# Kernel optimization log

Measured on AMD Instinct MI355X. Metric: run time of the kernel, lower is better.

## Reference

```python
import jax, jax.numpy as jnp
import numpy as np

B, N1, D, H = 64, 201, 128, 4
HALF = (N1 - 1) // 2  # 100 pickup/delivery pairs
V_RANGE = 6.0
NEG = -1e20


def _uni(key, shape):
    s = 1.0 / np.sqrt(shape[-1])
    return jax.random.uniform(key, shape, jnp.float32, -s, s)


def setup_inputs() -> dict:
    key = jax.random.key(0)
    ks = jax.random.split(key, 24)
    h_wave = jax.random.normal(ks[0], (B, N1, D), jnp.float32)
    # solution must be a valid permutation per batch (it is argsorted / self-gathered)
    solution = jax.vmap(lambda k: jax.random.permutation(k, N1))(jax.random.split(ks[1], B)).astype(jnp.int32)
    selection_recent = jax.random.uniform(ks[2], (B, 4, HALF), jnp.float32)
    pre_action = jax.random.randint(ks[3], (B, 2), 1, HALF).astype(jnp.int32)
    mask_table = jnp.zeros((B, N1, N1), dtype=bool)
    params = dict(
        Wn=_uni(ks[4], (D, D)), Wg=_uni(ks[5], (D, D)),
        rm_WQ=_uni(ks[6], (H, D, D)), rm_WK=_uni(ks[7], (H, D, D)),
        rm_w1=_uni(ks[8], (2 * H + 4, 32)), rm_b1=_uni(ks[9], (32,)),
        rm_w2=_uni(ks[10], (32, 32)), rm_b2=_uni(ks[11], (32,)),
        rm_w3=_uni(ks[12], (32, 1)), rm_b3=_uni(ks[13], (1,)),
        i1_Wq=_uni(ks[14], (H, D, D)), i1_Wk=_uni(ks[15], (H, D, D)),
        i2_Wq=_uni(ks[16], (H, D, D)), i2_Wk=_uni(ks[17], (H, D, D)),
        re_w1=_uni(ks[18], (4 * H, 32)), re_b1=_uni(ks[19], (32,)),
        re_w2=_uni(ks[20], (32, 32)), re_b2=_uni(ks[21], (32,)),
        re_w3=_uni(ks[22], (32, 1)), re_b3=_uni(ks[23], (1,)),
    )
    return dict(h_wave=h_wave, solution=solution, selection_recent=selection_recent,
                pre_action=pre_action, mask_table=mask_table, **params)


def _mlp(x, w1, b1, w2, b2, w3, b3):
    x = jax.nn.relu(x @ w1 + b1)
    x = jax.nn.relu(x @ w2 + b2)
    return (x @ w3 + b3)[..., 0]


def _mha_compat(q, k, Wq, Wk):
    # q: [B,Q,Din], k: [B,K,Din]; Wq/Wk: [H,Din,Dh] -> compat [H,B,Q,K]
    Q = jnp.einsum('bqd,hde->hbqe', q, Wq)
    K = jnp.einsum('bkd,hde->hbke', k, Wk)
    return jnp.einsum('hbqe,hbke->hbqk', Q, K) * (1.0 / np.sqrt(Wq.shape[-1]))


def _removal(h_hat, solution, selection_recent, WQ, WK, w1, b1, w2, b2, w3, b3):
    pre = jnp.argsort(solution, axis=1)
    post = jnp.take_along_axis(solution, solution, axis=1)
    hQ = jnp.einsum('bnd,hde->hbne', h_hat, WQ)  # [H,B,N1,D]
    hK = jnp.einsum('bnd,hde->hbne', h_hat, WK)
    Qpre = jnp.take_along_axis(hQ, pre[None, :, :, None], axis=2)
    Kpost = jnp.take_along_axis(hK, post[None, :, :, None], axis=2)
    comp = ((Qpre * hK).sum(-1) + (hQ * Kpost).sum(-1) - (Qpre * Kpost).sum(-1))[:, :, 1:]  # [H,B,N1-1]
    pairing = jnp.concatenate([comp[:, :, :N1 // 2], comp[:, :, N1 // 2:]], axis=0)  # [2H,B,HALF]
    feat = jnp.concatenate([jnp.transpose(pairing, (1, 2, 0)),
                            jnp.transpose(selection_recent, (0, 2, 1))], axis=-1)  # [B,HALF,2H+4]
    return _mlp(feat, w1, b1, w2, b2, w3, b3)  # [B,HALF]


def _reinsertion(h_hat, pos_pickup, pos_delivery, solution, Wq1, Wk1, Wq2, Wk2, w1, b1, w2, b2, w3, b3):
    ar = jnp.arange(B)
    h_p = h_hat[ar, pos_pickup][:, None, :]   # [B,1,D]
    h_d = h_hat[ar, pos_delivery][:, None, :]
    h_nb = jnp.take_along_axis(h_hat, solution[:, :, None], axis=1)  # [B,N1,D]

    def as_row(c):  # [H,B,1,N1] -> [B,N1,1,H] broadcast over columns
        return jnp.broadcast_to(jnp.transpose(c, (1, 2, 3, 0)).reshape(B, N1, 1, H), (B, N1, N1, H))

    def as_col(c):  # [H,B,1,N1] -> [B,1,N1,H] broadcast over rows
        return jnp.broadcast_to(jnp.transpose(c, (1, 2, 3, 0)).reshape(B, 1, N1, H), (B, N1, N1, H))

    feat = jnp.concatenate([
        as_row(_mha_compat(h_p, h_hat, Wq1, Wk1)),
        as_row(_mha_compat(h_p, h_nb, Wq2, Wk2)),
        as_col(_mha_compat(h_d, h_hat, Wq1, Wk1)),
        as_col(_mha_compat(h_d, h_nb, Wq2, Wk2)),
    ], axis=-1)  # [B,N1,N1,4H]
    return _mlp(feat, w1, b1, w2, b2, w3, b3)  # [B,N1,N1]


def _forward(h_wave, selection_recent, Wn, Wg, rm_WQ, rm_WK, rm_w1, rm_b1, rm_w2, rm_b2,
             rm_w3, rm_b3, i1_Wq, i1_Wk, i2_Wq, i2_Wk, re_w1, re_b1, re_w2, re_b2,
             re_w3, re_b3, solution, pre_action, mask_table):
    ar = jnp.arange(B)
    h_hat = h_wave @ Wn + (jnp.max(h_wave, axis=1) @ Wg)[:, None, :]
    t1 = jnp.tanh(_removal(h_hat, solution, selection_recent, rm_WQ, rm_WK,
                           rm_w1, rm_b1, rm_w2, rm_b2, rm_w3, rm_b3)) * V_RANGE
    t1 = jnp.where(pre_action[0, 0] > 0, t1.at[ar, pre_action[:, 0]].set(NEG), t1)
    logp1 = jax.nn.log_softmax(t1, axis=-1)
    a1 = jnp.argmax(t1, axis=-1)  # deterministic stand-in for Categorical sampling
    ll1 = jnp.take_along_axis(logp1, a1[:, None], axis=1)[:, 0]
    pos_pickup = 1 + a1
    pos_delivery = pos_pickup + HALF
    t2 = jnp.tanh(_reinsertion(h_hat, pos_pickup, pos_delivery, solution,
                               i1_Wq, i1_Wk, i2_Wq, i2_Wk,
                               re_w1, re_b1, re_w2, re_b2, re_w3, re_b3)) * V_RANGE
    t2 = jnp.where(mask_table, NEG, t2).reshape(B, N1 * N1)
    logp2 = jax.nn.log_softmax(t2, axis=-1)
    pair = jnp.argmax(t2, axis=-1)
    ll2 = jnp.take_along_axis(logp2, pair[:, None], axis=1)[:, 0]
    action = jnp.stack([a1, pair // N1, pair % N1], axis=-1)
    return action, ll1 + ll2


def reference(h_wave, solution, selection_recent, pre_action, mask_table,
              Wn, Wg, rm_WQ, rm_WK, rm_w1, rm_b1, rm_w2, rm_b2, rm_w3, rm_b3,
              i1_Wq, i1_Wk, i2_Wq, i2_Wk, re_w1, re_b1, re_w2, re_b2, re_w3, re_b3):
    return _forward(h_wave, selection_recent, Wn, Wg, rm_WQ, rm_WK, rm_w1, rm_b1,
                    rm_w2, rm_b2, rm_w3, rm_b3, i1_Wq, i1_Wk, i2_Wq, i2_Wk,
                    re_w1, re_b1, re_w2, re_b2, re_w3, re_b3,
                    solution, pre_action, mask_table)
```

## Files before the change

### kernel.cpp

```cpp
#include <hip/hip_runtime.h>
#include <math.h>

#define BB 64
#define N1 201
#define DD 128
#define HALF 100
#define NN (N1*N1)
#define NEGV (-1e20f)
#define QSCALE 0.08838834764831845f
#define NELE 1646592u

typedef __attribute__((ext_vector_type(8))) short short8v;
typedef __attribute__((ext_vector_type(4))) float float4v;

#define OFF_M    0u
#define OFF_MF   196608u
#define OFF_HWB  516096u
#define OFF_HHAT 2985984u
#define OFF_HBF  4632576u
#define OFF_G    7102464u
#define OFF_PMAX 7110656u
#define OFF_CMP  7143424u
#define OFF_Q    7194624u
#define OFF_ROWH 7325696u
#define OFF_COLH 7737344u
#define OFF_SC   8148992u
#define OFF_PM   8149248u
#define OFF_PS   8151296u
#define OFF_PI   8153344u
#define OFF_W2F  8155392u

__device__ __forceinline__ unsigned short f2bf(float x) {
    unsigned u = __float_as_uint(x);
    unsigned r = u + 0x7fffu + ((u >> 16) & 1u);
    return (unsigned short)(r >> 16);
}
__device__ __forceinline__ float bf2f(unsigned short h) {
    return __uint_as_float(((unsigned)h) << 16);
}

__global__ void kprep2(const float* __restrict__ rmWQ, const float* __restrict__ rmWK,
                       const float* __restrict__ i1Wq, const float* __restrict__ i1Wk,
                       const float* __restrict__ i2Wq, const float* __restrict__ i2Wk,
                       const float* __restrict__ re_w2, float* __restrict__ ws) {
    int m = blockIdx.x, jg = blockIdx.y, t = threadIdx.x;
    if (m == 12) {
        if (jg != 0) return;
        unsigned short* w2f = (unsigned short*)(ws + OFF_W2F);
        for (int idx = t; idx < 4*64*8; idx += 128) {
            int fs = idx >> 9, l = (idx >> 3) & 63, i = idx & 7;
            int j = 16*(fs >> 1) + (l & 15);
            int k = ((l >> 4) * 8) + i;
            float v = re_w2[k*32 + j];
            unsigned short hi = f2bf(v);
            unsigned short outv;
            if (fs & 1) outv = f2bf(v - bf2f(hi));
            else        outv = hi;
            w2f[idx] = outv;
        }
        return;
    }
    const float* WQ; const float* WK;
    if (m < 4)      { WQ = rmWQ + m*16384;     WK = rmWK + m*16384; }
    else if (m < 8) { WQ = i1Wq + (m-4)*16384; WK = i1Wk + (m-4)*16384; }
    else            { WQ = i2Wq + (m-8)*16384; WK = i2Wk + (m-8)*16384; }
    __shared__ float wq[128*132];
    __shared__ float wk[32*133];
    for (int idx = t; idx < 128*128; idx += 128) {
        int r = idx >> 7, e = idx & 127;
        wq[r*132 + e] = WQ[idx];
    }
    for (int idx = t; idx < 32*128; idx += 128) {
        int r = idx >> 7, e = idx & 127;
        wk[r*133 + e] = WK[(jg*32 + r)*128 + e];
    }
    __syncthreads();
    int j = t & 31, iq = t >> 5;
    for (int i2 = 0; i2 < 32; ++i2) {
        int i = iq*32 + i2;
        float acc = 0.f;
        #pragma unroll 8
        for (int e = 0; e < 128; ++e) acc += wq[i*132 + e]*wk[j*133 + e];
        ws[OFF_M + m*16384 + i*128 + jg*32 + j] = acc;
    }
}

__global__ void kfrag(const float* __restrict__ Wn, float* __restrict__ ws) {
    int bid = blockIdx.x;
    int mat = bid >> 5, rem = bid & 31, nt = rem >> 2, ks = rem & 3;
    const float* src = (mat < 12) ? (ws + OFF_M + mat*16384) : Wn;
    int l = threadIdx.x;
    unsigned short* mf = (unsigned short*)(ws + OFF_MF)
                       + (size_t)mat*49152 + (size_t)((nt*4 + ks)*3)*512 + l*8;
    #pragma unroll
    for (int i = 0; i < 8; ++i) {
        int k = ks*32 + (l >> 4)*8 + i;
        int col = nt*16 + (l & 15);
        float v = src[k*128 + col];
        unsigned short h = f2bf(v);
        float r1 = v - bf2f(h);
        unsigned short mm = f2bf(r1);
        unsigned short lo = f2bf(r1 - bf2f(mm));
        mf[i] = h; mf[512 + i] = mm; mf[1024 + i] = lo;
    }
}

__global__ void khw3(const float* __restrict__ hw, float* __restrict__ ws) {
    unsigned idx = blockIdx.x*256u + threadIdx.x;
    if (idx >= NELE) return;
    unsigned short* hh = (unsigned short*)(ws + OFF_HWB);
    unsigned short* hm = hh + NELE;
    unsigned short* hl = hh + 2u*NELE;
    float v = hw[idx];
    unsigned short a = f2bf(v);
    float r1 = v - bf2f(a);
    unsigned short b = f2bf(r1);
    unsigned short c = f2bf(r1 - bf2f(b));
    hh[idx] = a; hm[idx] = b; hl[idx] = c;
}

__global__ void kpartmax(const float* __restrict__ hw, float* __restrict__ pmax) {
    int b = blockIdx.x, p = blockIdx.y, d = threadIdx.x;
    int n0 = p*51, ne = n0 + 51; if (ne > N1) ne = N1;
    float m = -INFINITY;
    const float* src = hw + ((size_t)b*N1)*DD + d;
    for (int n = n0; n < ne; ++n) m = fmaxf(m, src[n*DD]);
    pmax[(b*4 + p)*128 + d] = m;
}

__global__ void khmaxg(const float* __restrict__ pmax, const float* __restrict__ Wg,
                       float* __restrict__ g) {
    int b = blockIdx.x, d = threadIdx.x;
    __shared__ float hm[128];
    const float* pm = pmax + b*4*128 + d;
    hm[d] = fmaxf(fmaxf(pm[0], pm[128]), fmaxf(pm[256], pm[384]));
    __syncthreads();
    float acc = 0.f;
    for (int k = 0; k < 128; ++k) acc += hm[k] * Wg[k*128 + d];
    g[b*128 + d] = acc;
}

__global__ __launch_bounds__(256) void khhat2(const float* __restrict__ g,
                                              float* __restrict__ ws) {
    int b = blockIdx.x, cg = blockIdx.y;
    int t = threadIdx.x, w = t >> 6, l = t & 63;
    const unsigned short* hwh = (const unsigned short*)(ws + OFF_HWB);
    const unsigned short* hwm = hwh + NELE;
    const unsigned short* hwl = hwh + 2u*NELE;
    const unsigned short* wnf = (const unsigned short*)(ws + OFF_MF) + (size_t)12*49152;
    float* hhat = ws + OFF_HHAT;
    unsigned short* hbh = (unsigned short*)(ws + OFF_HBF);
    unsigned short* hbm = hbh + NELE;
    unsigned short* hbl = hbh + 2u*NELE;
    int col0 = cg*32 + (l & 15);
    float g0 = g[b*128 + col0];
    float g1 = g[b*128 + col0 + 16];
    for (int mt = w; mt < 13; mt += 4) {
        int arow = mt*16 + (l & 15); if (arow > 200) arow = 200;
        size_t abase = ((size_t)b*N1 + arow)*DD;
        float4v acc0 = {g0, g0, g0, g0};
        float4v acc1 = {g1, g1, g1, g1};
        #pragma unroll
        for (int ks = 0; ks < 4; ++ks) {
            size_t ao = abase + ks*32 + (l >> 4)*8;
            short8v ah = *(const short8v*)(hwh + ao);
            short8v am = *(const short8v*)(hwm + ao);
            short8v al = *(const short8v*)(hwl + ao);
            const short8v* bf0 = (const short8v*)(wnf + (size_t)(((cg*2 + 0)*4 + ks)*3)*512) + l;
            const short8v* bf1 = (const short8v*)(wnf + (size_t)(((cg*2 + 1)*4 + ks)*3)*512) + l;
            short8v bh0 = bf0[0], bm0 = bf0[64], bl0 = bf0[128];
            short8v bh1 = bf1[0], bm1 = bf1[64], bl1 = bf1[128];
            acc0 = __builtin_amdgcn_mfma_f32_16x16x32_bf16(ah, bh0, acc0, 0, 0, 0);
            acc1 = __builtin_amdgcn_mfma_f32_16x16x32_bf16(ah, bh1, acc1, 0, 0, 0);
            acc0 = __builtin_amdgcn_mfma_f32_16x16x32_bf16(ah, bm0, acc0, 0, 0, 0);
            acc1 = __builtin_amdgcn_mfma_f32_16x16x32_bf16(ah, bm1, acc1, 0, 0, 0);
            acc0 = __builtin_amdgcn_mfma_f32_16x16x32_bf16(am, bh0, acc0, 0, 0, 0);
            acc1 = __builtin_amdgcn_mfma_f32_16x16x32_bf16(am, bh1, acc1, 0, 0, 0);
            acc0 = __builtin_amdgcn_mfma_f32_16x16x32_bf16(ah, bl0, acc0, 0, 0, 0);
            acc1 = __builtin_amdgcn_mfma_f32_16x16x32_bf16(ah, bl1, acc1, 0, 0, 0);
            acc0 = __builtin_amdgcn_mfma_f32_16x16x32_bf16(al, bh0, acc0, 0, 0, 0);
            acc1 = __builtin_amdgcn_mfma_f32_16x16x32_bf16(al, bh1, acc1, 0, 0, 0);
            acc0 = __builtin_amdgcn_mfma_f32_16x16x32_bf16(am, bm0, acc0, 0, 0, 0);
            acc1 = __builtin_amdgcn_mfma_f32_16x16x32_bf16(am, bm1, acc1, 0, 0, 0);
        }
        #pragma unroll
        for (int r = 0; r < 4; ++r) {
            int row = mt*16 + (l >> 4)*4 + r;
            if (row < N1) {
                size_t i0 = ((size_t)b*N1 + row)*DD + col0;
                float v0 = acc0[r], v1 = acc1[r];
                hhat[i0] = v0; hhat[i0 + 16] = v1;
                unsigned short a0 = f2bf(v0); float r10 = v0 - bf2f(a0);
                unsigned short b0 = f2bf(r10);
                hbh[i0] = a0; hbm[i0] = b0; hbl[i0] = f2bf(r10 - bf2f(b0));
                unsigned short a1 = f2bf(v1); float r11 = v1 - bf2f(a1);
                unsigned short b1 = f2bf(r11);
                hbh[i0+16] = a1; hbm[i0+16] = b1; hbl[i0+16] = f2bf(r11 - bf2f(b1));
            }
        }
    }
}

__global__ __launch_bounds__(256) void kAC(const int* __restrict__ solution,
                                           float* __restrict__ ws) {
    int b = blockIdx.x, h = blockIdx.y;
    int t = threadIdx.x, w = t >> 6, l = t & 63;
    __shared__ float As[N1*132];
    __shared__ int sol[N1], pre[N1], post[N1];
    if (t < N1) sol[t] = solution[b*N1 + t];
    __syncthreads();
    if (t < N1) { pre[sol[t]] = t; post[t] = sol[sol[t]]; }
    const unsigned short* hbh = (const unsigned short*)(ws + OFF_HBF);
    const unsigned short* hbm = hbh + NELE;
    const unsigned short* hbl = hbh + 2u*NELE;
    const unsigned short* mfm = (const unsigned short*)(ws + OFF_MF) + (size_t)h*49152;
    for (int mt = 0; mt < 13; ++mt) {
        int arow = mt*16 + (l & 15); if (arow > 200) arow = 200;
        size_t abase = ((size_t)b*N1 + arow)*DD;
        float4v acc0 = {0.f, 0.f, 0.f, 0.f};
        float4v acc1 = {0.f, 0.f, 0.f, 0.f};
        #pragma unroll
        for (int ks = 0; ks < 4; ++ks) {
            size_t ao = abase + ks*32 + (l >> 4)*8;
            short8v ah = *(const short8v*)(hbh + ao);
            short8v am = *(const short8v*)(hbm + ao);
            short8v al = *(const short8v*)(hbl + ao);
            const short8v* bf0 = (const short8v*)(mfm + (size_t)(((2*w + 0)*4 + ks)*3)*512) + l;
            const short8v* bf1 = (const short8v*)(mfm + (size_t)(((2*w + 1)*4 + ks)*3)*512) + l;
            short8v bh0 = bf0[0], bm0 = bf0[64], bl0 = bf0[128];
            short8v bh1 = bf1[0], bm1 = bf1[64], bl1 = bf1[128];
            acc0 = __builtin_amdgcn_mfma_f32_16x16x32_bf16(ah, bh0, acc0, 0, 0, 0);
            acc1 = __builtin_amdgcn_mfma_f32_16x16x32_bf16(ah, bh1, acc1, 0, 0, 0);
            acc0 = __builtin_amdgcn_mfma_f32_16x16x32_bf16(ah, bm0, acc0, 0, 0, 0);
            acc1 = __builtin_amdgcn_mfma_f32_16x16x32_bf16(ah, bm1, acc1, 0, 0, 0);
            acc0 = __builtin_amdgcn_mfma_f32_16x16x32_bf16(am, bh0, acc0, 0, 0, 0);
            acc1 = __builtin_amdgcn_mfma_f32_16x16x32_bf16(am, bh1, acc1, 0, 0, 0);
            acc0 = __builtin_amdgcn_mfma_f32_16x16x32_bf16(ah, bl0, acc0, 0, 0, 0);
            acc1 = __builtin_amdgcn_mfma_f32_16x16x32_bf16(ah, bl1, acc1, 0, 0, 0);
            acc0 = __builtin_amdgcn_mfma_f32_16x16x32_bf16(al, bh0, acc0, 0, 0, 0);
            acc1 = __builtin_amdgcn_mfma_f32_16x16x32_bf16(al, bh1, acc1, 0, 0, 0);
            acc0 = __builtin_amdgcn_mfma_f32_16x16x32_bf16(am, bm0, acc0, 0, 0, 0);
            acc1 = __builtin_amdgcn_mfma_f32_16x16x32_bf16(am, bm1, acc1, 0, 0, 0);
        }
        #pragma unroll
        for (int r = 0; r < 4; ++r) {
            int row = mt*16 + (l >> 4)*4 + r;
            if (row < N1) {
                int col = 2*w*16 + (l & 15);
                As[row*132 + col] = acc0[r];
                As[row*132 + col + 16] = acc1[r];
            }
        }
    }
    __syncthreads();
    const float2* X = (const float2*)(ws + OFF_HHAT) + (size_t)b*N1*64;
    float* cmp = ws + OFF_CMP + (h*64 + b)*200;
    for (int n = 1 + w; n <= 200; n += 4) {
        int pn = pre[n], po = post[n];
        float2 xn = X[n*64 + l], xp = X[po*64 + l];
        float2 ap = *(const float2*)&As[pn*132 + 2*l];
        float2 an = *(const float2*)&As[n*132 + 2*l];
        float v = ap.x*(xn.x - xp.x) + ap.y*(xn.y - xp.y) + an.x*xp.x + an.y*xp.y;
        #pragma unroll
        for (int off = 32; off; off >>= 1) v += __shfl_xor(v, off);
        if (l == 0) cmp[n - 1] = v;
    }
}

__global__ void krm2(const float* __restrict__ sel, const int* __restrict__ pre_action,
                     const float* __restrict__ w1, const float* __restrict__ b1,
                     const float* __restrict__ w2, const float* __restrict__ b2,
                     const float* __restrict__ w3, const float* __restrict__ b3,
                     const float* __restrict__ cmpg, float* __restrict__ sc) {
    int b = blockIdx.x, t = threadIdx.x;
    __shared__ float t1l[100];
    if (t < 100) {
        float f[12];
        #pragma unroll
        for (int h = 0; h < 4; ++h) {
            f[h]     = cmpg[(h*64 + b)*200 + t];
            f[4 + h] = cmpg[(h*64 + b)*200 + 100 + t];
        }
        #pragma unroll
        for (int s = 0; s < 4; ++s) f[8 + s] = sel[b*400 + s*100 + t];
        float h1[32];
        #pragma unroll
        for (int k = 0; k < 32; ++k) h1[k] = b1[k];
        #pragma unroll
        for (int j = 0; j < 12; ++j) {
            const float* wr = w1 + j*32;
            #pragma unroll
            for (int k = 0; k < 32; ++k) h1[k] += f[j]*wr[k];
        }
        #pragma unroll
        for (int k = 0; k < 32; ++k) h1[k] = fmaxf(h1[k], 0.f);
        float acc[32];
        #pragma unroll
        for (int j = 0; j < 32; ++j) acc[j] = b2[j];
        #pragma unroll
        for (int k = 0; k < 32; ++k) {
            const float* wr = w2 + k*32;
            #pragma unroll
            for (int j = 0; j < 32; ++j) acc[j] += h1[k]*wr[j];
        }
        float out = b3[0];
        #pragma unroll
        for (int j = 0; j < 32; ++j) out += fmaxf(acc[j], 0.f)*w3[j];
        t1l[t] = tanhf(out)*6.0f;
    }
    __syncthreads();
    if (t == 0) {
        if (pre_action[0] > 0) t1l[pre_action[b*2]] = NEGV;
        float M = -INFINITY; int a1 = 0;
        for (int i = 0; i < 100; ++i) if (t1l[i] > M) { M = t1l[i]; a1 = i; }
        float S = 0.f;
        for (int i = 0; i < 100; ++i) S += __expf(t1l[i] - M);
        int* ia = (int*)sc;
        ia[b] = a1; ia[64 + b] = 1 + a1; ia[128 + b] = 101 + a1;
        sc[192 + b] = -__logf(S);
    }
}

__global__ void kqvec(const float* __restrict__ Mall, const float* __restrict__ hhat,
                      const float* __restrict__ sc, float* __restrict__ q) {
    int b = blockIdx.x, h = blockIdx.y, j = threadIdx.x;
    const int* ia = (const int*)sc;
    int pp = ia[64 + b], pd = ia[128 + b];
    __shared__ float xp[128], xd[128];
    const float* hb = hhat + (size_t)b*N1*DD;
    xp[j] = hb[pp*DD + j];
    xd[j] = hb[pd*DD + j];
    __syncthreads();
    const float* M1 = Mall + (4 + h)*16384;
    const float* M2 = Mall + (8 + h)*16384;
    float a1p = 0, a2p = 0, a1d = 0, a2d = 0;
    for (int i = 0; i < 128; ++i) {
        float w1v = M1[i*128 + j], w2v = M2[i*128 + j];
        a1p += xp[i]*w1v; a1d += xd[i]*w1v;
        a2p += xp[i]*w2v; a2d += xd[i]*w2v;
    }
    q[((0*4 + h)*64 + b)*128 + j] = a1p*QSCALE;
    q[((1*4 + h)*64 + b)*128 + j] = a2p*QSCALE;
    q[((2*4 + h)*64 + b)*128 + j] = a1d*QSCALE;
    q[((3*4 + h)*64 + b)*128 + j] = a2d*QSCALE;
}

__global__ void krowcol(const int* __restrict__ solution, const float* __restrict__ w1,
                        const float* __restrict__ b1, const float* __restrict__ qg,
                        const float* __restrict__ hhat, float* __restrict__ rowH,
                        float* __restrict__ colH) {
    int b = blockIdx.x, ch = blockIdx.y, t = threadIdx.x;
    int n = ch*51 + t;
    int ne = ch*51 + 51; if (ne > N1) ne = N1;
    if (n >= ne || t >= 51) return;
    int sn = solution[b*N1 + n];
    const float* ra = hhat + ((size_t)b*N1 + n)*DD;
    const float* rb = hhat + ((size_t)b*N1 + sn)*DD;
    float cv[16];
    #pragma unroll
    for (int j = 0; j < 16; ++j) cv[j] = 0.f;
    for (int ec = 0; ec < 4; ++ec) {
        float xa[32], xb[32];
        #pragma unroll
        for (int q4 = 0; q4 < 8; ++q4) {
            float4 va = ((const float4*)(ra + ec*32))[q4];
            float4 vb = ((const float4*)(rb + ec*32))[q4];
            xa[q4*4+0]=va.x; xa[q4*4+1]=va.y; xa[q4*4+2]=va.z; xa[q4*4+3]=va.w;
            xb[q4*4+0]=vb.x; xb[q4*4+1]=vb.y; xb[q4*4+2]=vb.z; xb[q4*4+3]=vb.w;
        }
        #pragma unroll
        for (int j = 0; j < 16; ++j) {
            const float* qp = qg + ((size_t)j*64 + b)*128 + ec*32;
            int kind = j >> 2;
            float a = 0.f;
            if (kind & 1) {
                #pragma unroll
                for (int e = 0; e < 32; ++e) a += qp[e]*xb[e];
            } else {
                #pragma unroll
                for (int e = 0; e < 32; ++e) a += qp[e]*xa[e];
            }
            cv[j] += a;
        }
    }
    float* rO = rowH + ((size_t)b*N1 + n)*32;
    float* cO = colH + ((size_t)b*N1 + n)*32;
    #pragma unroll
    for (int k = 0; k < 32; ++k) {
        float rh = b1[k], chh = 0.f;
        #pragma unroll
        for (int j = 0; j < 8; ++j)  rh  += cv[j]*w1[j*32 + k];
        #pragma unroll
        for (int j = 8; j < 16; ++j) chh += cv[j]*w1[j*32 + k];
        rO[k] = rh; cO[k] = chh;
    }
}

__global__ __launch_bounds__(64) void kt2(
        const unsigned char* __restrict__ maskt,
        const float* __restrict__ rowH, const float* __restrict__ colH,
        const unsigned short* __restrict__ w2f,
        const float* __restrict__ b2g, const float* __restrict__ w3g,
        const float* __restrict__ b3g,
        float* __restrict__ pm, float* __restrict__ ps, int* __restrict__ pi) {
    int b = blockIdx.x, cy = blockIdx.y, rz = blockIdx.z;
    int l = threadIdx.x;
    int c0 = cy*64;
    int r0 = rz*26, rend = r0 + 26; if (rend > N1) rend = N1;
    int rcnt = rend - r0;
    __shared__ float colc[64*36];
    __shared__ float rowr[26*36];

    const short8v* wf = (const short8v*)w2f;
    short8v w2hi0 = wf[0*64 + l];
    short8v w2lo0 = wf[1*64 + l];
    short8v w2hi1 = wf[2*64 + l];
    short8v w2lo1 = wf[3*64 + l];
    int sg = l >> 4;
    float4v b2f0 = *(const float4v*)(b2g + sg*4);
    float4v b2f1 = *(const float4v*)(b2g + 16 + sg*4);
    float4v w3f0 = *(const float4v*)(w3g + sg*4);
    float4v w3f1 = *(const float4v*)(w3g + 16 + sg*4);
    float b3v = b3g[0];

    {
        int cg = c0 + l;
        float4v* dst = (float4v*)(colc + l*36);
        if (cg < N1) {
            const float4v* src = (const float4v*)(colH + ((size_t)b*N1 + cg)*32);
            #pragma unroll
            for (int q = 0; q < 8; ++q) dst[q] = src[q];
        } else {
            float4v z = {0.f, 0.f, 0.f, 0.f};
            #pragma unroll
            for (int q = 0; q < 8; ++q) dst[q] = z;
        }
    }
    for (int idx = l; idx < rcnt*32; idx += 64) {
        int rr = idx >> 5, k = idx & 31;
        rowr[rr*36 + k] = rowH[((size_t)b*N1 + r0 + rr)*32 + k];
    }
    __syncthreads();

    float m = -INFINITY, s = 0.f;
    int mi = 0x7fffffff;
    int c = c0 + l;
    bool valid = c < N1;
    const unsigned char* mrow = maskt + (size_t)b*NN + c0 + (l < 64 ? l : 0);

    for (int rr = 0; rr < rcnt; ++rr) {
        int r = r0 + rr;
        const float4v* rp = (const float4v*)(rowr + rr*36 + sg*8);
        float4v ra = rp[0], rb = rp[1];
        float outv = 0.f;
        #pragma unroll
        for (int g = 0; g < 4; ++g) {
            const float4v* cp = (const float4v*)(colc + (16*g + (l & 15))*36 + sg*8);
            float4v ca = cp[0], cb = cp[1];
            float h[8];
            #pragma unroll
            for (int e = 0; e < 4; ++e) {
                h[e]   = fmaxf(ra[e] + ca[e], 0.f);
                h[4+e] = fmaxf(rb[e] + cb[e], 0.f);
            }
            short8v bh, bl;
            #pragma unroll
            for (int e = 0; e < 8; ++e) {
                unsigned short hb = f2bf(h[e]);
                bh[e] = (short)hb;
                bl[e] = (short)f2bf(h[e] - bf2f(hb));
            }
            float4v a0 = b2f0, a1 = b2f1;
            a0 = __builtin_amdgcn_mfma_f32_16x16x32_bf16(w2hi0, bh, a0, 0, 0, 0);
            a0 = __builtin_amdgcn_mfma_f32_16x16x32_bf16(w2hi0, bl, a0, 0, 0, 0);
            a0 = __builtin_amdgcn_mfma_f32_16x16x32_bf16(w2lo0, bh, a0, 0, 0, 0);
            a0 = __builtin_amdgcn_mfma_f32_16x16x32_bf16(w2lo0, bl, a0, 0, 0, 0);
            a1 = __builtin_amdgcn_mfma_f32_16x16x32_bf16(w2hi1, bh, a1, 0, 0, 0);
            a1 = __builtin_amdgcn_mfma_f32_16x16x32_bf16(w2hi1, bl, a1, 0, 0, 0);
            a1 = __builtin_amdgcn_mfma_f32_16x16x32_bf16(w2lo1, bh, a1, 0, 0, 0);
            a1 = __builtin_amdgcn_mfma_f32_16x16x32_bf16(w2lo1, bl, a1, 0, 0, 0);
            float p = 0.f;
            #pragma unroll
            for (int reg = 0; reg < 4; ++reg) {
                p += fmaxf(a0[reg], 0.f)*w3f0[reg];
                p += fmaxf(a1[reg], 0.f)*w3f1[reg];
            }
            p += __shfl_xor(p, 16);
            p += __shfl_xor(p, 32);
            if (sg == g) outv = p + b3v;
        }
        float ex = __expf(2.f*outv);
        float tv = 6.f - 12.f/(ex + 1.f);
        if (mrow[(size_t)r*N1]) tv = NEGV;
        if (valid) {
            if (tv > m) { s = s*__expf(m - tv) + 1.f; m = tv; mi = r*N1 + c; }
            else        { s += __expf(tv - m); }
        }
    }
    #pragma unroll
    for (int off = 1; off < 64; off <<= 1) {
        float om = __shfl_xor(m, off);
        float os = __shfl_xor(s, off);
        int oi = __shfl_xor(mi, off);
        float M2 = fmaxf(m, om);
        float sn = (s > 0.f ? s*__expf(m - M2) : 0.f)
                 + (os > 0.f ? os*__expf(om - M2) : 0.f);
        int in_;
        if (m > om) in_ = mi; else if (om > m) in_ = oi; else in_ = (mi < oi ? mi : oi);
        m = M2; s = sn; mi = in_;
    }
    if (l == 0) {
        int slot = b*32 + cy*8 + rz;
        pm[slot] = m; ps[slot] = s; pi[slot] = mi;
    }
}

__global__ void kfinal(float* __restrict__ out, const float* __restrict__ pm,
                       const float* __restrict__ ps, const int* __restrict__ pi,
                       const float* __restrict__ sc) {
    int b = blockIdx.x, lane = threadIdx.x;
    float m = -INFINITY, s = 0.f;
    int mi = 0x7fffffff;
    if (lane < 32) {
        m = pm[b*32 + lane];
        s = ps[b*32 + lane];
        mi = pi[b*32 + lane];
    }
    #pragma unroll
    for (int off = 1; off < 64; off <<= 1) {
        float om = __shfl_xor(m, off);
        float os = __shfl_xor(s, off);
        int oi = __shfl_xor(mi, off);
        float M2 = fmaxf(m, om);
        float sn = (s > 0.f ? s*__expf(m - M2) : 0.f)
                 + (os > 0.f ? os*__expf(om - M2) : 0.f);
        int in_;
        if (m > om) in_ = mi; else if (om > m) in_ = oi; else in_ = (mi < oi ? mi : oi);
        m = M2; s = sn; mi = in_;
    }
    if (lane == 0) {
        float ll2 = -__logf(s);
        const int* ia = (const int*)sc;
        out[b*3 + 0] = (float)ia[b];
        out[b*3 + 1] = (float)(mi / N1);
        out[b*3 + 2] = (float)(mi % N1);
        out[192 + b] = sc[192 + b] + ll2;
    }
}

extern "C" void kernel_launch(void* const* d_in, const int* in_sizes, int n_in,
                              void* d_out, int out_size, void* d_ws, size_t ws_size,
                              hipStream_t stream) {
    const float* h_wave    = (const float*)d_in[0];
    const int*   solution  = (const int*)d_in[1];
    const float* sel       = (const float*)d_in[2];
    const int*   pre_act   = (const int*)d_in[3];
    const unsigned char* maskt = (const unsigned char*)d_in[4];
    const float* Wn    = (const float*)d_in[5];
    const float* Wg    = (const float*)d_in[6];
    const float* rmWQ  = (const float*)d_in[7];
    const float* rmWK  = (const float*)d_in[8];
    const float* rm_w1 = (const float*)d_in[9];
    const float* rm_b1 = (const float*)d_in[10];
    const float* rm_w2 = (const float*)d_in[11];
    const float* rm_b2 = (const float*)d_in[12];
    const float* rm_w3 = (const float*)d_in[13];
    const float* rm_b3 = (const float*)d_in[14];
    const float* i1Wq  = (const float*)d_in[15];
    const float* i1Wk  = (const float*)d_in[16];
    const float* i2Wq  = (const float*)d_in[17];
    const float* i2Wk  = (const float*)d_in[18];
    const float* re_w1 = (const float*)d_in[19];
    const float* re_b1 = (const float*)d_in[20];
    const float* re_w2 = (const float*)d_in[21];
    const float* re_b2 = (const float*)d_in[22];
    const float* re_w3 = (const float*)d_in[23];
    const float* re_b3 = (const float*)d_in[24];
    float* ws = (float*)d_ws;
    float* out = (float*)d_out;

    kprep2<<<dim3(13, 4), dim3(128), 0, stream>>>(rmWQ, rmWK, i1Wq, i1Wk, i2Wq, i2Wk,
                                                  re_w2, ws);
    kfrag<<<dim3(416), dim3(64), 0, stream>>>(Wn, ws);
    khw3<<<dim3(6432), dim3(256), 0, stream>>>(h_wave, ws);
    kpartmax<<<dim3(64, 4), dim3(128), 0, stream>>>(h_wave, ws + OFF_PMAX);
    khmaxg<<<dim3(64), dim3(128), 0, stream>>>(ws + OFF_PMAX, Wg, ws + OFF_G);
    khhat2<<<dim3(64, 4), dim3(256), 0, stream>>>(ws + OFF_G, ws);
    kAC<<<dim3(64, 4), dim3(256), 0, stream>>>(solution, ws);
    krm2<<<dim3(64), dim3(128), 0, stream>>>(sel, pre_act, rm_w1, rm_b1, rm_w2, rm_b2,
                                             rm_w3, rm_b3, ws + OFF_CMP, ws + OFF_SC);
    kqvec<<<dim3(64, 4), dim3(128), 0, stream>>>(ws + OFF_M, ws + OFF_HHAT,
                                                 ws + OFF_SC, ws + OFF_Q);
    krowcol<<<dim3(64, 4), dim3(64), 0, stream>>>(solution, re_w1, re_b1,
                                                  ws + OFF_Q, ws + OFF_HHAT,
                                                  ws + OFF_ROWH, ws + OFF_COLH);
    kt2<<<dim3(64, 4, 8), dim3(64), 0, stream>>>(maskt, ws + OFF_ROWH, ws + OFF_COLH,
                                                 (const unsigned short*)(ws + OFF_W2F),
                                                 re_b2, re_w3, re_b3,
                                                 ws + OFF_PM, ws + OFF_PS,
                                                 (int*)(ws + OFF_PI));
    kfinal<<<dim3(64), dim3(64), 0, stream>>>(out, ws + OFF_PM, ws + OFF_PS,
                                              (const int*)(ws + OFF_PI), ws + OFF_SC);
}
```

Baseline: 363.1 us.

## Merge small kernels, widen grids, and use packed bf16 conversion in scoring

Several launch-level changes are combined. The weight-product prep kernel now spreads over a 12x4x4 grid instead of 13x4, and the re_w2 fragment packing moves into kfrag. The partial-max plus gating pair and the removal-MLP plus q-vector pair are each fused into one kernel, which cuts four launches to two. The t2 scoring grid doubles its row splits to 16 for more parallelism, and kfinal now reduces 64 partials. The manual bf16 hi/lo split is replaced by packed v_cvt_pk_bf16_f32 instructions. The trade-off is that the fused kernels run fewer, more serial blocks: khmaxg2 scans all 201 rows per block, and krmq loops over 4 heads in one block.

```diff
diff --git a/kernel.cpp b/kernel.cpp
--- a/kernel.cpp
+++ b/kernel.cpp
@@ -19,16 +19,15 @@
 #define OFF_HHAT 2985984u
 #define OFF_HBF  4632576u
 #define OFF_G    7102464u
-#define OFF_PMAX 7110656u
-#define OFF_CMP  7143424u
-#define OFF_Q    7194624u
-#define OFF_ROWH 7325696u
-#define OFF_COLH 7737344u
-#define OFF_SC   8148992u
-#define OFF_PM   8149248u
-#define OFF_PS   8151296u
-#define OFF_PI   8153344u
-#define OFF_W2F  8155392u
+#define OFF_CMP  7110656u
+#define OFF_Q    7161856u
+#define OFF_ROWH 7292928u
+#define OFF_COLH 7704576u
+#define OFF_SC   8116224u
+#define OFF_PM   8116480u
+#define OFF_PS   8120576u
+#define OFF_PI   8124672u
+#define OFF_W2F  8128768u
 
 __device__ __forceinline__ unsigned short f2bf(float x) {
     unsigned u = __float_as_uint(x);
@@ -42,54 +41,49 @@
 __global__ void kprep2(const float* __restrict__ rmWQ, const float* __restrict__ rmWK,
                        const float* __restrict__ i1Wq, const float* __restrict__ i1Wk,
                        const float* __restrict__ i2Wq, const float* __restrict__ i2Wk,
-                       const float* __restrict__ re_w2, float* __restrict__ ws) {
-    int m = blockIdx.x, jg = blockIdx.y, t = threadIdx.x;
-    if (m == 12) {
-        if (jg != 0) return;
-        unsigned short* w2f = (unsigned short*)(ws + OFF_W2F);
-        for (int idx = t; idx < 4*64*8; idx += 128) {
-            int fs = idx >> 9, l = (idx >> 3) & 63, i = idx & 7;
-            int j = 16*(fs >> 1) + (l & 15);
-            int k = ((l >> 4) * 8) + i;
-            float v = re_w2[k*32 + j];
-            unsigned short hi = f2bf(v);
-            unsigned short outv;
-            if (fs & 1) outv = f2bf(v - bf2f(hi));
-            else        outv = hi;
-            w2f[idx] = outv;
-        }
-        return;
-    }
+                       float* __restrict__ ws) {
+    int m = blockIdx.x, ig = blockIdx.y, jg = blockIdx.z, t = threadIdx.x;
     const float* WQ; const float* WK;
     if (m < 4)      { WQ = rmWQ + m*16384;     WK = rmWK + m*16384; }
     else if (m < 8) { WQ = i1Wq + (m-4)*16384; WK = i1Wk + (m-4)*16384; }
     else            { WQ = i2Wq + (m-8)*16384; WK = i2Wk + (m-8)*16384; }
-    __shared__ float wq[128*132];
+    __shared__ float wq[32*132];
     __shared__ float wk[32*133];
-    for (int idx = t; idx < 128*128; idx += 128) {
-        int r = idx >> 7, e = idx & 127;
-        wq[r*132 + e] = WQ[idx];
-    }
     for (int idx = t; idx < 32*128; idx += 128) {
         int r = idx >> 7, e = idx & 127;
+        wq[r*132 + e] = WQ[(ig*32 + r)*128 + e];
         wk[r*133 + e] = WK[(jg*32 + r)*128 + e];
     }
     __syncthreads();
     int j = t & 31, iq = t >> 5;
-    for (int i2 = 0; i2 < 32; ++i2) {
-        int i = iq*32 + i2;
+    #pragma unroll
+    for (int i2 = 0; i2 < 8; ++i2) {
+        int i = iq*8 + i2;
         float acc = 0.f;
         #pragma unroll 8
         for (int e = 0; e < 128; ++e) acc += wq[i*132 + e]*wk[j*133 + e];
-        ws[OFF_M + m*16384 + i*128 + jg*32 + j] = acc;
-    }
-}
-
-__global__ void kfrag(const float* __restrict__ Wn, float* __restrict__ ws) {
+        ws[OFF_M + m*16384 + (ig*32 + i)*128 + jg*32 + j] = acc;
+    }
+}
+
+__global__ void kfrag(const float* __restrict__ Wn, const float* __restrict__ re_w2,
+                      float* __restrict__ ws) {
     int bid = blockIdx.x;
+    int l = threadIdx.x;
+    if (bid == 416) {
+        unsigned short* w2f = (unsigned short*)(ws + OFF_W2F);
+        for (int idx = l; idx < 2048; idx += 64) {
+            int fs = idx >> 9, ll = (idx >> 3) & 63, i = idx & 7;
+            int j = 16*(fs >> 1) + (ll & 15);
+            int k = ((ll >> 4)*8) + i;
+            float v = re_w2[k*32 + j];
+            unsigned short hi = f2bf(v);
+            w2f[idx] = (fs & 1) ? f2bf(v - bf2f(hi)) : hi;
+        }
+        return;
+    }
     int mat = bid >> 5, rem = bid & 31, nt = rem >> 2, ks = rem & 3;
     const float* src = (mat < 12) ? (ws + OFF_M + mat*16384) : Wn;
-    int l = threadIdx.x;
     unsigned short* mf = (unsigned short*)(ws + OFF_MF)
                        + (size_t)mat*49152 + (size_t)((nt*4 + ks)*3)*512 + l*8;
     #pragma unroll
@@ -119,21 +113,14 @@
     hh[idx] = a; hm[idx] = b; hl[idx] = c;
 }
 
-__global__ void kpartmax(const float* __restrict__ hw, float* __restrict__ pmax) {
-    int b = blockIdx.x, p = blockIdx.y, d = threadIdx.x;
-    int n0 = p*51, ne = n0 + 51; if (ne > N1) ne = N1;
-    float m = -INFINITY;
-    const float* src = hw + ((size_t)b*N1)*DD + d;
-    for (int n = n0; n < ne; ++n) m = fmaxf(m, src[n*DD]);
-    pmax[(b*4 + p)*128 + d] = m;
-}
-
-__global__ void khmaxg(const float* __restrict__ pmax, const float* __restrict__ Wg,
-                       float* __restrict__ g) {
+__global__ void khmaxg2(const float* __restrict__ hw, const float* __restrict__ Wg,
+                        float* __restrict__ g) {
     int b = blockIdx.x, d = threadIdx.x;
     __shared__ float hm[128];
-    const float* pm = pmax + b*4*128 + d;
-    hm[d] = fmaxf(fmaxf(pm[0], pm[128]), fmaxf(pm[256], pm[384]));
+    float m = -INFINITY;
+    const float* src = hw + (size_t)b*N1*DD + d;
+    for (int n = 0; n < N1; ++n) m = fmaxf(m, src[n*DD]);
+    hm[d] = m;
     __syncthreads();
     float acc = 0.f;
     for (int k = 0; k < 128; ++k) acc += hm[k] * Wg[k*128 + d];
@@ -267,13 +254,17 @@
     }
 }
 
-__global__ void krm2(const float* __restrict__ sel, const int* __restrict__ pre_action,
+__global__ void krmq(const float* __restrict__ sel, const int* __restrict__ pre_action,
                      const float* __restrict__ w1, const float* __restrict__ b1,
                      const float* __restrict__ w2, const float* __restrict__ b2,
                      const float* __restrict__ w3, const float* __restrict__ b3,
-                     const float* __restrict__ cmpg, float* __restrict__ sc) {
+                     const float* __restrict__ Mall, const float* __restrict__ hhat,
+                     const float* __restrict__ cmpg, float* __restrict__ sc,
+                     float* __restrict__ q) {
     int b = blockIdx.x, t = threadIdx.x;
     __shared__ float t1l[100];
+    __shared__ int ppd[2];
+    __shared__ float xp[128], xd[128];
     if (t < 100) {
         float f[12];
         #pragma unroll
@@ -316,33 +307,32 @@
         float S = 0.f;
         for (int i = 0; i < 100; ++i) S += __expf(t1l[i] - M);
         int* ia = (int*)sc;
-        ia[b] = a1; ia[64 + b] = 1 + a1; ia[128 + b] = 101 + a1;
+        ia[b] = a1;
         sc[192 + b] = -__logf(S);
-    }
-}
-
-__global__ void kqvec(const float* __restrict__ Mall, const float* __restrict__ hhat,
-                      const float* __restrict__ sc, float* __restrict__ q) {
-    int b = blockIdx.x, h = blockIdx.y, j = threadIdx.x;
-    const int* ia = (const int*)sc;
-    int pp = ia[64 + b], pd = ia[128 + b];
-    __shared__ float xp[128], xd[128];
+        ppd[0] = 1 + a1; ppd[1] = 101 + a1;
+    }
+    __syncthreads();
+    int pp = ppd[0], pd = ppd[1];
     const float* hb = hhat + (size_t)b*N1*DD;
-    xp[j] = hb[pp*DD + j];
-    xd[j] = hb[pd*DD + j];
-    __syncthreads();
-    const float* M1 = Mall + (4 + h)*16384;
-    const float* M2 = Mall + (8 + h)*16384;
-    float a1p = 0, a2p = 0, a1d = 0, a2d = 0;
-    for (int i = 0; i < 128; ++i) {
-        float w1v = M1[i*128 + j], w2v = M2[i*128 + j];
-        a1p += xp[i]*w1v; a1d += xd[i]*w1v;
-        a2p += xp[i]*w2v; a2d += xd[i]*w2v;
-    }
-    q[((0*4 + h)*64 + b)*128 + j] = a1p*QSCALE;
-    q[((1*4 + h)*64 + b)*128 + j] = a2p*QSCALE;
-    q[((2*4 + h)*64 + b)*128 + j] = a1d*QSCALE;
-    q[((3*4 + h)*64 + b)*128 + j] = a2d*QSCALE;
+    xp[t] = hb[pp*DD + t];
+    xd[t] = hb[pd*DD + t];
+    __syncthreads();
+    int j = t;
+    #pragma unroll
+    for (int h = 0; h < 4; ++h) {
+        const float* M1 = Mall + (4 + h)*16384;
+        const float* M2 = Mall + (8 + h)*16384;
+        float a1p = 0, a2p = 0, a1d = 0, a2d = 0;
+        for (int i = 0; i < 128; ++i) {
+            float w1v = M1[i*128 + j], w2v = M2[i*128 + j];
+            a1p += xp[i]*w1v; a1d += xd[i]*w1v;
+            a2p += xp[i]*w2v; a2d += xd[i]*w2v;
+        }
+        q[((0*4 + h)*64 + b)*128 + j] = a1p*QSCALE;
+        q[((1*4 + h)*64 + b)*128 + j] = a2p*QSCALE;
+        q[((2*4 + h)*64 + b)*128 + j] = a1d*QSCALE;
+        q[((3*4 + h)*64 + b)*128 + j] = a2d*QSCALE;
+    }
 }
 
 __global__ void krowcol(const int* __restrict__ solution, const float* __restrict__ w1,
@@ -406,10 +396,10 @@
     int b = blockIdx.x, cy = blockIdx.y, rz = blockIdx.z;
     int l = threadIdx.x;
     int c0 = cy*64;
-    int r0 = rz*26, rend = r0 + 26; if (rend > N1) rend = N1;
+    int r0 = rz*13, rend = r0 + 13; if (rend > N1) rend = N1;
     int rcnt = rend - r0;
     __shared__ float colc[64*36];
-    __shared__ float rowr[26*36];
+    __shared__ float rowr[13*36];
 
     const short8v* wf = (const short8v*)w2f;
     short8v w2hi0 = wf[0*64 + l];
@@ -446,7 +436,9 @@
     int mi = 0x7fffffff;
     int c = c0 + l;
     bool valid = c < N1;
-    const unsigned char* mrow = maskt + (size_t)b*NN + c0 + (l < 64 ? l : 0);
+    const unsigned char* mrow = maskt + (size_t)b*NN + c0 + l;
+
+    union U8 { unsigned u[4]; short8v s8; };
 
     for (int rr = 0; rr < rcnt; ++rr) {
         int r = r0 + rr;
@@ -463,13 +455,18 @@
                 h[e]   = fmaxf(ra[e] + ca[e], 0.f);
                 h[4+e] = fmaxf(rb[e] + cb[e], 0.f);
             }
-            short8v bh, bl;
-            #pragma unroll
-            for (int e = 0; e < 8; ++e) {
-                unsigned short hb = f2bf(h[e]);
-                bh[e] = (short)hb;
-                bl[e] = (short)f2bf(h[e] - bf2f(hb));
+            U8 B, L;
+            #pragma unroll
+            for (int e = 0; e < 4; ++e) {
+                unsigned ph, pl;
+                asm("v_cvt_pk_bf16_f32 %0, %1, %2" : "=v"(ph) : "v"(h[2*e]), "v"(h[2*e+1]));
+                float h0 = __uint_as_float(ph << 16);
+                float h1f = __uint_as_float(ph & 0xffff0000u);
+                float l0 = h[2*e] - h0, l1 = h[2*e+1] - h1f;
+                asm("v_cvt_pk_bf16_f32 %0, %1, %2" : "=v"(pl) : "v"(l0), "v"(l1));
+                B.u[e] = ph; L.u[e] = pl;
             }
+            short8v bh = B.s8, bl = L.s8;
             float4v a0 = b2f0, a1 = b2f1;
             a0 = __builtin_amdgcn_mfma_f32_16x16x32_bf16(w2hi0, bh, a0, 0, 0, 0);
             a0 = __builtin_amdgcn_mfma_f32_16x16x32_bf16(w2hi0, bl, a0, 0, 0, 0);
@@ -510,7 +507,7 @@
         m = M2; s = sn; mi = in_;
     }
     if (l == 0) {
-        int slot = b*32 + cy*8 + rz;
+        int slot = b*64 + cy*16 + rz;
         pm[slot] = m; ps[slot] = s; pi[slot] = mi;
     }
 }
@@ -519,13 +516,9 @@
                        const float* __restrict__ ps, const int* __restrict__ pi,
                        const float* __restrict__ sc) {
     int b = blockIdx.x, lane = threadIdx.x;
-    float m = -INFINITY, s = 0.f;
-    int mi = 0x7fffffff;
-    if (lane < 32) {
-        m = pm[b*32 + lane];
-        s = ps[b*32 + lane];
-        mi = pi[b*32 + lane];
-    }
+    float m = pm[b*64 + lane];
+    float s = ps[b*64 + lane];
+    int mi = pi[b*64 + lane];
     #pragma unroll
     for (int off = 1; off < 64; off <<= 1) {
         float om = __shfl_xor(m, off);
@@ -579,26 +572,23 @@
     float* ws = (float*)d_ws;
     float* out = (float*)d_out;
 
-    kprep2<<<dim3(13, 4), dim3(128), 0, stream>>>(rmWQ, rmWK, i1Wq, i1Wk, i2Wq, i2Wk,
-                                                  re_w2, ws);
-    kfrag<<<dim3(416), dim3(64), 0, stream>>>(Wn, ws);
+    kprep2<<<dim3(12, 4, 4), dim3(128), 0, stream>>>(rmWQ, rmWK, i1Wq, i1Wk, i2Wq, i2Wk, ws);
+    kfrag<<<dim3(417), dim3(64), 0, stream>>>(Wn, re_w2, ws);
     khw3<<<dim3(6432), dim3(256), 0, stream>>>(h_wave, ws);
-    kpartmax<<<dim3(64, 4), dim3(128), 0, stream>>>(h_wave, ws + OFF_PMAX);
-    khmaxg<<<dim3(64), dim3(128), 0, stream>>>(ws + OFF_PMAX, Wg, ws + OFF_G);
+    khmaxg2<<<dim3(64), dim3(128), 0, stream>>>(h_wave, Wg, ws + OFF_G);
     khhat2<<<dim3(64, 4), dim3(256), 0, stream>>>(ws + OFF_G, ws);
     kAC<<<dim3(64, 4), dim3(256), 0, stream>>>(solution, ws);
-    krm2<<<dim3(64), dim3(128), 0, stream>>>(sel, pre_act, rm_w1, rm_b1, rm_w2, rm_b2,
-                                             rm_w3, rm_b3, ws + OFF_CMP, ws + OFF_SC);
-    kqvec<<<dim3(64, 4), dim3(128), 0, stream>>>(ws + OFF_M, ws + OFF_HHAT,
-                                                 ws + OFF_SC, ws + OFF_Q);
+    krmq<<<dim3(64), dim3(128), 0, stream>>>(sel, pre_act, rm_w1, rm_b1, rm_w2, rm_b2,
+                                             rm_w3, rm_b3, ws + OFF_M, ws + OFF_HHAT,
+                                             ws + OFF_CMP, ws + OFF_SC, ws + OFF_Q);
     krowcol<<<dim3(64, 4), dim3(64), 0, stream>>>(solution, re_w1, re_b1,
                                                   ws + OFF_Q, ws + OFF_HHAT,
                                                   ws + OFF_ROWH, ws + OFF_COLH);
-    kt2<<<dim3(64, 4, 8), dim3(64), 0, stream>>>(maskt, ws + OFF_ROWH, ws + OFF_COLH,
-                                                 (const unsigned short*)(ws + OFF_W2F),
-                                                 re_b2, re_w3, re_b3,
-                                                 ws + OFF_PM, ws + OFF_PS,
-                                                 (int*)(ws + OFF_PI));
+    kt2<<<dim3(64, 4, 16), dim3(64), 0, stream>>>(maskt, ws + OFF_ROWH, ws + OFF_COLH,
+                                                  (const unsigned short*)(ws + OFF_W2F),
+                                                  re_b2, re_w3, re_b3,
+                                                  ws + OFF_PM, ws + OFF_PS,
+                                                  (int*)(ws + OFF_PI));
     kfinal<<<dim3(64), dim3(64), 0, stream>>>(out, ws + OFF_PM, ws + OFF_PS,
                                               (const int*)(ws + OFF_PI), ws + OFF_SC);
 }
```

Result: faster. 354.5 us (-2.4%).
